# Performance work log

Measured on AMD Instinct MI355X. Metric: run time of the kernel, lower is better.

## Reference

```python
import jax, jax.numpy as jnp
import numpy as np

N = 20000          # nodes
E = 640000         # edges
IN_F, CL1_F, CL2_F, OUT_F = 128, 256, 128, 10
K = 4              # Chebyshev order
EPS = 1e-5         # BatchNorm eps
LAMBDA_MAX = 2.0   # PyG ChebConv default


def setup_inputs() -> dict:
    key = jax.random.key(0)
    ks = jax.random.split(key, 8)
    x = jax.random.normal(ks[0], (N, IN_F), dtype=jnp.float32)
    edge_index = jax.random.randint(ks[1], (2, E), 0, N, dtype=jnp.int64)
    edge_weight = jax.random.uniform(ks[2], (E,), dtype=jnp.float32)
    W1 = jax.random.normal(ks[3], (K, IN_F, CL1_F), dtype=jnp.float32) * 0.05
    b1 = jnp.zeros((CL1_F,), jnp.float32)
    W2 = jax.random.normal(ks[4], (K, CL1_F, CL2_F), dtype=jnp.float32) * 0.05
    b2 = jnp.zeros((CL2_F,), jnp.float32)
    gamma1 = jnp.ones((CL1_F,), jnp.float32); beta1 = jnp.zeros((CL1_F,), jnp.float32)
    gamma2 = jnp.ones((CL2_F,), jnp.float32); beta2 = jnp.zeros((CL2_F,), jnp.float32)
    Wlin = jax.random.normal(ks[5], (OUT_F, CL2_F), dtype=jnp.float32) * 0.05
    blin = jnp.zeros((OUT_F,), jnp.float32)
    return {"x": x, "edge_index": edge_index, "edge_weight": edge_weight,
            "W1": W1, "b1": b1, "W2": W2, "b2": b2,
            "gamma1": gamma1, "beta1": beta1, "gamma2": gamma2, "beta2": beta2,
            "Wlin": Wlin, "blin": blin}


def _cheb_norm(edge_index, edge_weight, n):
    # Scaled Laplacian L_hat = (2/lambda_max) * (I - D^{-1/2} A D^{-1/2}) - I
    # (matches PyG ChebConv __norm__ with normalization='sym').
    row, col = edge_index[0], edge_index[1]
    w = jnp.where(row == col, 0.0, edge_weight)  # remove_self_loops
    deg = jax.ops.segment_sum(w, row, num_segments=n)
    dis = jnp.where(deg > 0, 1.0 / jnp.sqrt(deg), 0.0)
    w_norm = -(dis[row] * w * dis[col]) * (2.0 / LAMBDA_MAX)
    diag_w = 2.0 / LAMBDA_MAX - 1.0  # = 0 for lambda_max=2
    return row, col, w_norm, diag_w


def _cheb_conv(x, row, col, w_norm, diag_w, W, b):
    n = x.shape[0]

    def spmm(t):  # L_hat @ t : gather sources, scale, scatter-add to targets
        return jax.ops.segment_sum(w_norm[:, None] * t[row], col, num_segments=n) + diag_w * t

    Tx0 = x
    out = Tx0 @ W[0]
    Tx1 = spmm(Tx0)
    out = out + Tx1 @ W[1]
    for k in range(2, W.shape[0]):  # Chebyshev recursion T_k = 2 L_hat T_{k-1} - T_{k-2}
        Tx2 = 2.0 * spmm(Tx1) - Tx0
        out = out + Tx2 @ W[k]
        Tx0, Tx1 = Tx1, Tx2
    return out + b


def _batchnorm(x, gamma, beta):  # training-mode BN over the node axis
    m = x.mean(axis=0)
    v = x.var(axis=0)
    return gamma * (x - m) / jnp.sqrt(v + EPS) + beta


def reference(x, edge_index, edge_weight, W1, b1, W2, b2,
              gamma1, beta1, gamma2, beta2, Wlin, blin):
    row, col, w_norm, diag_w = _cheb_norm(edge_index, edge_weight, x.shape[0])
    h = jax.nn.relu(_cheb_conv(x, row, col, w_norm, diag_w, W1, b1))
    h = _batchnorm(h, gamma1, beta1)
    h = jax.nn.relu(_cheb_conv(h, row, col, w_norm, diag_w, W2, b2))
    h = _batchnorm(h, gamma2, beta2)
    return h @ Wlin.T + blin  # [N, OUT_F]
```

## Files before the change

kernel.cpp:

```cpp
#include <hip/hip_runtime.h>
#include <cstdint>
#include <cstddef>

#define NNODES 20000
#define NEDGES 640000
#define IN_F   128
#define CL1_F  256
#define CL2_F  128
#define OUT_F  10
#define BN_EPS 1e-5f

#define NC     256
#define CE     (NEDGES / NC)
#define HALFN  10000

#define WB1    512
#define WB2    512
#define XB     ((NNODES * 16) / 256)

typedef unsigned short u16;


__device__ __forceinline__ float bf2f(u16 u) {
    union { uint32_t i; float f; } v; v.i = ((uint32_t)u) << 16; return v.f;
}
__device__ __forceinline__ u16 f2bf(float f) {
    union { float f; uint32_t i; } v; v.f = f;
    uint32_t r = v.i + 0x7fffu + ((v.i >> 16) & 1u);
    return (u16)(r >> 16);
}
__device__ __forceinline__ void bf2x2(uint32_t u, float& lo, float& hi) {
    union { uint32_t i; float f; } a, b;
    a.i = u << 16; b.i = u & 0xffff0000u;
    lo = a.f; hi = b.f;
}
__device__ __forceinline__ uint32_t f2bf2(float lo, float hi) {
    return (uint32_t)f2bf(lo) | ((uint32_t)f2bf(hi) << 16);
}
__device__ __forceinline__ void unpack8(uint4 v, float* o) {
    bf2x2(v.x, o[0], o[1]); bf2x2(v.y, o[2], o[3]);
    bf2x2(v.z, o[4], o[5]); bf2x2(v.w, o[6], o[7]);
}


__launch_bounds__(256)
__global__ void build_hist_conv(const int* __restrict__ ei, const float* __restrict__ ew,
                                u16* __restrict__ cnt_h, u16* __restrict__ degq_h,
                                const float* __restrict__ W1, u16* __restrict__ W1t,
                                const float* __restrict__ W2, u16* __restrict__ W2t,
                                const float* __restrict__ x, u16* __restrict__ A1,
                                int E, int N) {
    __shared__ uint32_t scnt[HALFN / 2];
    __shared__ uint32_t sdeg[HALFN / 2];
    int b = blockIdx.x;
    if (b < NC) {
        int e0 = b * CE, e1 = e0 + CE;
        for (int half = 0; half < 2; ++half) {
            int lo = half * HALFN;
            for (int i = threadIdx.x; i < HALFN / 2; i += 256) { scnt[i] = 0; sdeg[i] = 0; }
            __syncthreads();
            for (int e = e0 + threadIdx.x; e < e1; e += 256) {
                int r = ei[e];
                int c = ei[E + e];
                int ci = c - lo;
                if ((unsigned)ci < HALFN) atomicAdd(&scnt[ci >> 1], 1u << ((ci & 1) * 16));
                int ri = r - lo;
                if ((unsigned)ri < HALFN) {
                    float w = (r == c) ? 0.0f : ew[e];
                    uint32_t q = (uint32_t)(w * 1024.0f + 0.5f);
                    atomicAdd(&sdeg[ri >> 1], q << ((ri & 1) * 16));
                }
            }
            __syncthreads();
            for (int i = threadIdx.x; i < HALFN; i += 256) {
                cnt_h[(size_t)b * N + lo + i]  = (u16)((scnt[i >> 1] >> ((i & 1) * 16)) & 0xffffu);
                degq_h[(size_t)b * N + lo + i] = (u16)((sdeg[i >> 1] >> ((i & 1) * 16)) & 0xffffu);
            }
            __syncthreads();
        }
    } else {
        int b2 = b - NC;
        if (b2 < WB1) {
            int i = b2 * 256 + threadIdx.x;
            int k = i >> 8, n = i & 255;
            W1t[(size_t)n * 512 + k] = f2bf(W1[i]);
        } else if (b2 < WB1 + WB2) {
            int j = (b2 - WB1) * 256 + threadIdx.x;
            int kc = j / (256 * 128);
            int rem = j - kc * 256 * 128;
            int ci = rem >> 7, co = rem & 127;
            W2t[(size_t)(kc * 128 + co) * 256 + ci] = f2bf(W2[j]);
        } else {
            int j = (b2 - WB1 - WB2) * 256 + threadIdx.x;
            int n = j >> 4, f = (j & 15) << 3;
            const float4* xp = (const float4*)(x + (size_t)n * 128 + f);
            float4 v0 = xp[0], v1 = xp[1];
            uint4 o;
            o.x = f2bf2(v0.x, v0.y); o.y = f2bf2(v0.z, v0.w);
            o.z = f2bf2(v1.x, v1.y); o.w = f2bf2(v1.z, v1.w);
            *(uint4*)(A1 + (size_t)n * 512 + f) = o;
        }
    }
}

__global__ void reduce_dis_base(const u16* __restrict__ cnt_h, const u16* __restrict__ degq_h,
                                int* __restrict__ tot, float* __restrict__ dis,
                                u16* __restrict__ baseD, int N) {
    int i = blockIdx.x * blockDim.x + threadIdx.x;
    if (i >= N) return;
    int t = 0;
    uint32_t dq = 0;
#pragma unroll 8
    for (int c = 0; c < NC; ++c) {
        baseD[(size_t)c * N + i] = (u16)t;
        t  += cnt_h[(size_t)c * N + i];
        dq += degq_h[(size_t)c * N + i];
    }
    tot[i] = t;
    float d = (float)dq * (1.0f / 1024.0f);
    dis[i] = (d > 0.0f) ? rsqrtf(d) : 0.0f;
}


#define SCHUNK  80
#define SSTRIDE 81

__launch_bounds__(256)
__global__ void scan_kernel(const int* __restrict__ tot, int* __restrict__ rowptr, int N) {
    __shared__ int s[250 * SSTRIDE];
    __shared__ int wtot[4];
    int tid = threadIdx.x;

    const int4* t4 = (const int4*)tot;
    for (int i4 = tid; i4 < N / 4; i4 += 256) {
        int4 v = t4[i4];
        int i = i4 * 4;
        int c = i / SCHUNK;
        int idx = c * SSTRIDE + (i - c * SCHUNK);
        s[idx] = v.x; s[idx + 1] = v.y; s[idx + 2] = v.z; s[idx + 3] = v.w;
    }
    __syncthreads();

    int tsum = 0;
    if (tid < 250) {
        int base = tid * SSTRIDE;
#pragma unroll 8
        for (int j = 0; j < SCHUNK; ++j) tsum += s[base + j];
    }

    int lane = tid & 63, wv = tid >> 6;
    int pre = tsum;
#pragma unroll
    for (int off = 1; off < 64; off <<= 1) {
        int v = __shfl_up(pre, off);
        if (lane >= off) pre += v;
    }
    if (lane == 63) wtot[wv] = pre;
    __syncthreads();
    int run = pre - tsum;
    for (int w = 0; w < wv; ++w) run += wtot[w];
    if (tid == 0) rowptr[N] = wtot[0] + wtot[1] + wtot[2] + wtot[3];

    if (tid < 250) {
        int base = tid * SSTRIDE;
        for (int j = 0; j < SCHUNK; ++j) { int v = s[base + j]; s[base + j] = run; run += v; }
    }
    __syncthreads();

    int4* r4 = (int4*)rowptr;
    for (int i4 = tid; i4 < N / 4; i4 += 256) {
        int i = i4 * 4;
        int c = i / SCHUNK;
        int idx = c * SSTRIDE + (i - c * SCHUNK);
        int4 v;
        v.x = s[idx]; v.y = s[idx + 1]; v.z = s[idx + 2]; v.w = s[idx + 3];
        r4[i4] = v;
    }
}

__launch_bounds__(256)
__global__ void fill_kernel(const int* __restrict__ ei, const float* __restrict__ ew,
                            const float* __restrict__ dis, const int* __restrict__ rowptr,
                            const u16* __restrict__ baseD,
                            uint32_t* __restrict__ erec, int E, int N) {
    __shared__ uint32_t srank[NNODES / 2];
    int chunk = blockIdx.x;
    int e0 = chunk * CE, e1 = e0 + CE;
    for (int i = threadIdx.x; i < NNODES / 2; i += 256) srank[i] = 0;
    __syncthreads();
    for (int e = e0 + threadIdx.x; e < e1; e += 256) {
        int r = ei[e];
        int c = ei[E + e];
        float w = (r == c) ? 0.0f : ew[e];
        float wn = -(dis[r] * w * dis[c]);
        int sh = (c & 1) * 16;
        uint32_t old = atomicAdd(&srank[c >> 1], 1u << sh);
        int rank = (old >> sh) & 0xffff;
        int pos = rowptr[c] + (int)baseD[(size_t)chunk * N + c] + rank;
        erec[pos] = (uint32_t)r | ((uint32_t)f2bf(wn) << 16);
    }
}

__launch_bounds__(256)
__global__ void spmm_cl(const int* __restrict__ rowptr, const uint32_t* __restrict__ erec,
                        const u16* __restrict__ tin, int ldi,
                        const u16* __restrict__ t1, int ld1, float c1,
                        const u16* __restrict__ t2, int ld2, float c2,
                        u16* __restrict__ tout, int ldo,
                        const float* __restrict__ bias, int doReluBias,
                        int N, float s) {
    int gid = blockIdx.x * blockDim.x + threadIdx.x;
    int n = gid >> 4;
    if (n >= N) return;
    int f = (gid & 15) << 3;
    int p = rowptr[n], pe = rowptr[n + 1];
    float acc[8] = {};
    for (; p + 7 < pe; p += 8) {
        uint32_t rr[8];
#pragma unroll
        for (int u = 0; u < 8; ++u) rr[u] = erec[p + u];
        uint4 vv[8];
#pragma unroll
        for (int u = 0; u < 8; ++u)
            vv[u] = *(const uint4*)(tin + (size_t)(rr[u] & 0xffffu) * ldi + f);
#pragma unroll
        for (int u = 0; u < 8; ++u) {
            float w = bf2f((u16)(rr[u] >> 16));
            float fa[8];
            unpack8(vv[u], fa);
#pragma unroll
            for (int q = 0; q < 8; ++q) acc[q] += w * fa[q];
        }
    }
    for (; p < pe; ++p) {
        uint32_t r0 = erec[p];
        uint4 v0 = *(const uint4*)(tin + (size_t)(r0 & 0xffffu) * ldi + f);
        float w0 = bf2f((u16)(r0 >> 16));
        float fa[8];
        unpack8(v0, fa);
#pragma unroll
        for (int q = 0; q < 8; ++q) acc[q] += w0 * fa[q];
    }
#pragma unroll
    for (int q = 0; q < 8; ++q) acc[q] *= s;
    if (t1) {
        uint4 v = *(const uint4*)(t1 + (size_t)n * ld1 + f);
        float fv[8]; unpack8(v, fv);
#pragma unroll
        for (int q = 0; q < 8; ++q) acc[q] += c1 * fv[q];
    }
    if (t2) {
        uint4 v = *(const uint4*)(t2 + (size_t)n * ld2 + f);
        float fv[8]; unpack8(v, fv);
#pragma unroll
        for (int q = 0; q < 8; ++q) acc[q] += c2 * fv[q];
    }
    if (doReluBias) {
#pragma unroll
        for (int q = 0; q < 8; ++q) acc[q] = fmaxf(acc[q] + bias[f + q], 0.0f);
    }
    uint4 o;
    o.x = f2bf2(acc[0], acc[1]);
    o.y = f2bf2(acc[2], acc[3]);
    o.z = f2bf2(acc[4], acc[5]);
    o.w = f2bf2(acc[6], acc[7]);
    *(uint4*)(tout + (size_t)n * ldo + f) = o;
}


typedef __attribute__((ext_vector_type(8))) short short8;
typedef __attribute__((ext_vector_type(4))) float floatx4;

#define GBM 64
#define GBN 64
#define GBK 64

__launch_bounds__(256)
__global__ void gemm_mfma(const u16* __restrict__ A, const u16* __restrict__ Bt,
                          const float* __restrict__ bias, void* __restrict__ Cout,
                          float* __restrict__ ssum, float* __restrict__ ssq,
                          int M, int N, int K, int doRelu, int outBf) {
    __shared__ __align__(16) u16 As[GBM][GBK + 8];
    __shared__ __align__(16) u16 Bs[GBN][GBK + 8];
    __shared__ float colsum[GBN], colsq[GBN];

    int tid = threadIdx.x;
    int lane = tid & 63;
    int wave = tid >> 6;
    int wm = (wave & 1) * 32;
    int wn = (wave >> 1) * 32;
    int rowBase = blockIdx.x * GBM;
    int colBase = blockIdx.y * GBN;

    floatx4 acc[2][2];
#pragma unroll
    for (int i = 0; i < 2; ++i)
#pragma unroll
        for (int j = 0; j < 2; ++j) {
            acc[i][j][0] = 0.f; acc[i][j][1] = 0.f; acc[i][j][2] = 0.f; acc[i][j][3] = 0.f;
        }

    int sr = tid >> 3;
    int sc = (tid & 7) * 8;

    for (int k0 = 0; k0 < K; k0 += GBK) {
#pragma unroll
        for (int h = 0; h < 2; ++h) {
            int r = sr + h * 32;
            int gm = rowBase + r;
            uint4 v = make_uint4(0, 0, 0, 0);
            if (gm < M) v = *(const uint4*)(A + (size_t)gm * K + k0 + sc);
            *(uint4*)&As[r][sc] = v;
            int gn = colBase + r;
            uint4 w = *(const uint4*)(Bt + (size_t)gn * K + k0 + sc);
            *(uint4*)&Bs[r][sc] = w;
        }
        __syncthreads();

        int mrow = lane & 15;
        int kq = (lane >> 4) * 8;
#pragma unroll
        for (int kk = 0; kk < GBK; kk += 32) {
            short8 af[2], bfr[2];
#pragma unroll
            for (int i = 0; i < 2; ++i) af[i] = *(const short8*)&As[wm + i * 16 + mrow][kk + kq];
#pragma unroll
            for (int j = 0; j < 2; ++j) bfr[j] = *(const short8*)&Bs[wn + j * 16 + mrow][kk + kq];
#pragma unroll
            for (int i = 0; i < 2; ++i)
#pragma unroll
                for (int j = 0; j < 2; ++j)
                    acc[i][j] = __builtin_amdgcn_mfma_f32_16x16x32_bf16(af[i], bfr[j], acc[i][j], 0, 0, 0);
        }
        __syncthreads();
    }

    if (ssum) {
        if (tid < GBN) { colsum[tid] = 0.f; colsq[tid] = 0.f; }
        __syncthreads();
    }

    int cn0 = colBase + wn + (lane & 15);
    int rq = (lane >> 4) * 4;
    float* Cf = (float*)Cout;
    u16*   Cb = (u16*)Cout;
#pragma unroll
    for (int j = 0; j < 2; ++j) {
        float ps = 0.f, pq = 0.f;
        int n = cn0 + j * 16;
#pragma unroll
        for (int i = 0; i < 2; ++i) {
#pragma unroll
            for (int r = 0; r < 4; ++r) {
                int m = rowBase + wm + i * 16 + rq + r;
                if (m >= M) continue;
                float v = acc[i][j][r];
                if (bias) v += bias[n];
                if (doRelu) v = fmaxf(v, 0.0f);
                if (outBf) {
                    u16 bb = f2bf(v);
                    Cb[(size_t)m * N + n] = bb;
                    if (ssum) { float vb = bf2f(bb); ps += vb; pq += vb * vb; }
                } else {
                    Cf[(size_t)m * N + n] = v;
                }
            }
        }
        if (ssum) {
            int lc = wn + j * 16 + (lane & 15);
            atomicAdd(&colsum[lc], ps);
            atomicAdd(&colsq[lc], pq);
        }
    }
    if (ssum) {
        __syncthreads();
        if (tid < GBN) {
            atomicAdd(&ssum[colBase + tid], colsum[tid]);
            atomicAdd(&ssq[colBase + tid], colsq[tid]);
        }
    }
}


#define BN_ROWS 64
__global__ void bn_stats_bf(const u16* __restrict__ h, int N, int C,
                            float* __restrict__ sums, float* __restrict__ sumsq) {
    int c = threadIdx.x;
    int r0 = blockIdx.x * BN_ROWS;
    int r1 = min(r0 + BN_ROWS, N);
    float s = 0.f, q = 0.f;
    for (int r = r0; r < r1; ++r) {
        float v = bf2f(h[(size_t)r * C + c]);
        s += v;
        q += v * v;
    }
    atomicAdd(&sums[c], s);
    atomicAdd(&sumsq[c], q);
}

__launch_bounds__(256)
__global__ void fold_w2(u16* __restrict__ W2t, const float* __restrict__ sums,
                        const float* __restrict__ sumsq, const float* __restrict__ gamma,
                        const float* __restrict__ beta, float* __restrict__ rowvec, float invN) {
    __shared__ float red[4];
    int n = blockIdx.x;
    int k = threadIdx.x;
    float m = sums[k] * invN;
    float var = sumsq[k] * invN - m * m;
    float sc = gamma[k] / sqrtf(var + BN_EPS);
    float sh = beta[k] - m * sc;
    float wf = bf2f(W2t[(size_t)n * 256 + k]);
    W2t[(size_t)n * 256 + k] = f2bf(wf * sc);
    float part = sh * wf;
#pragma unroll
    for (int off = 32; off > 0; off >>= 1) part += __shfl_down(part, off);
    if ((k & 63) == 0) red[k >> 6] = part;
    __syncthreads();
    if (k == 0) rowvec[n] = red[0] + red[1] + red[2] + red[3];
}


__launch_bounds__(256)
__global__ void final_linear_bn(const u16* __restrict__ g, const float* __restrict__ Wlin,
                                const float* __restrict__ blin, const float* __restrict__ sums,
                                const float* __restrict__ sumsq, const float* __restrict__ gamma,
                                const float* __restrict__ beta, float* __restrict__ out,
                                int N, float invN) {
    __shared__ float Ws2[OUT_F][CL2_F + 4];
    __shared__ float scs[CL2_F], shs[CL2_F];
    __shared__ float oc[OUT_F];
    int tid = threadIdx.x;
    if (tid < CL2_F) {
        float m = sums[tid] * invN;
        float var = sumsq[tid] * invN - m * m;
        float sc = gamma[tid] / sqrtf(var + BN_EPS);
        scs[tid] = sc;
        shs[tid] = beta[tid] - m * sc;
    }
    __syncthreads();
    for (int i = tid; i < OUT_F * CL2_F; i += 256) {
        int f = i & 127;
        Ws2[i >> 7][f] = Wlin[i] * scs[f];
    }
    __syncthreads();
    if (tid < OUT_F) {
        float a = blin[tid];
        const float* wr = Wlin + tid * CL2_F;
        for (int f = 0; f < CL2_F; ++f) a += shs[f] * wr[f];
        oc[tid] = a;
    }
    __syncthreads();
    int idx = blockIdx.x * 256 + tid;
    if (idx >= N * OUT_F) return;
    int n = idx / OUT_F, o = idx - n * OUT_F;
    const u16* gr = g + (size_t)n * CL2_F;
    const float* w2 = Ws2[o];
    float acc = 0.f;
#pragma unroll
    for (int f0 = 0; f0 < CL2_F; f0 += 8) {
        uint4 v = *(const uint4*)(gr + f0);
        float fa[8]; unpack8(v, fa);
        const float4* wp = (const float4*)(w2 + f0);
        float4 wa = wp[0], wb = wp[1];
        acc += fa[0] * wa.x + fa[1] * wa.y + fa[2] * wa.z + fa[3] * wa.w
             + fa[4] * wb.x + fa[5] * wb.y + fa[6] * wb.z + fa[7] * wb.w;
    }
    out[idx] = acc + oc[o];
}


extern "C" void kernel_launch(void* const* d_in, const int* in_sizes, int n_in,
                              void* d_out, int out_size, void* d_ws, size_t ws_size,
                              hipStream_t stream) {
    const float* x      = (const float*)d_in[0];
    const int*   ei     = (const int*)d_in[1];
    const float* ew     = (const float*)d_in[2];
    const float* W1     = (const float*)d_in[3];
    const float* b1     = (const float*)d_in[4];
    const float* W2     = (const float*)d_in[5];
    const float* b2     = (const float*)d_in[6];
    const float* gamma1 = (const float*)d_in[7];
    const float* beta1  = (const float*)d_in[8];
    const float* gamma2 = (const float*)d_in[9];
    const float* beta2  = (const float*)d_in[10];
    const float* Wlin   = (const float*)d_in[11];
    const float* blin   = (const float*)d_in[12];
    float* out = (float*)d_out;

    const int N = NNODES, E = NEDGES;

    char* base = (char*)d_ws;
    u16*     cnt_h  = (u16*)    (base + 0);
    u16*     degq_h = (u16*)    (base + 10240000);
    u16*     baseD  = (u16*)    (base + 20480000);
    u16*     A1     = (u16*)    (base + 30720000);
    u16*     Hc     = A1;
    u16*     h1bf   = (u16*)    (base + 51200000);
    u16*     pbuf   = (u16*)    (base + 61440000);
    u16*     bb2    = (u16*)    (base + 66560000);
    u16*     bb1    = (u16*)    (base + 71680000);
    uint32_t* erec  = (uint32_t*)(base + 76800000);
    u16*     W1t    = (u16*)    (base + 79360000);
    u16*     W2t    = (u16*)    (base + 79622144);
    float*   rowvec = (float*)  (base + 79884288);
    int*     rowptr = (int*)    (base + 79886336);
    int*     tot    = (int*)    (base + 79966352);
    float*   dis    = (float*)  (base + 80046352);
    float*   bns1   = (float*)  (base + 80126352);
    float*   bnq1    = bns1 + 256;
    float*   bns2    = bnq1 + 256;
    float*   bnq2    = bns2 + 256;

    dim3 blk(256);

    hipMemsetAsync(bns1, 0, 4 * 256 * sizeof(float), stream);

    build_hist_conv<<<dim3(NC + WB1 + WB2 + XB), blk, 0, stream>>>(
        ei, ew, cnt_h, degq_h, W1, W1t, W2, W2t, x, A1, E, N);
    reduce_dis_base<<<dim3((N + 255) / 256), blk, 0, stream>>>(cnt_h, degq_h, tot, dis, baseD, N);
    scan_kernel<<<dim3(1), blk, 0, stream>>>(tot, rowptr, N);
    fill_kernel<<<dim3(NC), blk, 0, stream>>>(ei, ew, dis, rowptr, baseD, erec, E, N);

    dim3 gS(((N << 4) + 255) / 256);

    spmm_cl<<<gS, blk, 0, stream>>>(rowptr, erec, A1 + 0,   512, nullptr,  512, 0.f,
                                    nullptr, 512, 0.f, A1 + 128, 512, nullptr, 0, N, 1.0f);
    spmm_cl<<<gS, blk, 0, stream>>>(rowptr, erec, A1 + 128, 512, A1 + 0,   512, -1.f,
                                    nullptr, 512, 0.f, A1 + 256, 512, nullptr, 0, N, 2.0f);
    spmm_cl<<<gS, blk, 0, stream>>>(rowptr, erec, A1 + 256, 512, A1 + 128, 512, -1.f,
                                    nullptr, 512, 0.f, A1 + 384, 512, nullptr, 0, N, 2.0f);

    gemm_mfma<<<dim3((N + GBM - 1) / GBM, CL1_F / GBN), blk, 0, stream>>>(
        A1, W1t, b1, h1bf, bns1, bnq1, N, CL1_F, 512, 1, 1);

    fold_w2<<<dim3(512), dim3(256), 0, stream>>>(W2t, bns1, bnq1, gamma1, beta1, rowvec, 1.0f / N);

    gemm_mfma<<<dim3((N + GBM - 1) / GBM, 512 / GBN), blk, 0, stream>>>(
        h1bf, W2t, rowvec, Hc, nullptr, nullptr, N, 512, 256, 0, 1);

    spmm_cl<<<gS, blk, 0, stream>>>(rowptr, erec, Hc + 384, 512, Hc + 256, 512, 1.f,
                                    nullptr, 512, 0.f, bb2, 128, nullptr, 0, N, 2.0f);
    spmm_cl<<<gS, blk, 0, stream>>>(rowptr, erec, bb2, 128, Hc + 384, 512, -1.f,
                                    Hc + 128, 512, 1.f, bb1, 128, nullptr, 0, N, 2.0f);
    spmm_cl<<<gS, blk, 0, stream>>>(rowptr, erec, bb1, 128, bb2, 128, -1.f,
                                    Hc + 0, 512, 1.f, pbuf, 128, b2, 1, N, 1.0f);

    bn_stats_bf<<<dim3((N + BN_ROWS - 1) / BN_ROWS), dim3(CL2_F), 0, stream>>>(pbuf, N, CL2_F, bns2, bnq2);

    final_linear_bn<<<dim3((N * OUT_F + 255) / 256), blk, 0, stream>>>(
        pbuf, Wlin, blin, bns2, bnq2, gamma2, beta2, out, N, 1.0f / N);
}
```

Before: 349.6 us.

## Use float global atomics for degree, shuffle-shared edge loads in SpMM, vectorize BN stats

```diff
diff --git a/kernel.cpp b/kernel.cpp
--- a/kernel.cpp
+++ b/kernel.cpp
@@ -45,36 +45,31 @@
 
 __launch_bounds__(256)
 __global__ void build_hist_conv(const int* __restrict__ ei, const float* __restrict__ ew,
-                                u16* __restrict__ cnt_h, u16* __restrict__ degq_h,
+                                u16* __restrict__ cnt_h, float* __restrict__ degf,
                                 const float* __restrict__ W1, u16* __restrict__ W1t,
                                 const float* __restrict__ W2, u16* __restrict__ W2t,
                                 const float* __restrict__ x, u16* __restrict__ A1,
                                 int E, int N) {
     __shared__ uint32_t scnt[HALFN / 2];
-    __shared__ uint32_t sdeg[HALFN / 2];
     int b = blockIdx.x;
     if (b < NC) {
         int e0 = b * CE, e1 = e0 + CE;
         for (int half = 0; half < 2; ++half) {
             int lo = half * HALFN;
-            for (int i = threadIdx.x; i < HALFN / 2; i += 256) { scnt[i] = 0; sdeg[i] = 0; }
+            for (int i = threadIdx.x; i < HALFN / 2; i += 256) scnt[i] = 0;
             __syncthreads();
             for (int e = e0 + threadIdx.x; e < e1; e += 256) {
-                int r = ei[e];
                 int c = ei[E + e];
                 int ci = c - lo;
                 if ((unsigned)ci < HALFN) atomicAdd(&scnt[ci >> 1], 1u << ((ci & 1) * 16));
-                int ri = r - lo;
-                if ((unsigned)ri < HALFN) {
-                    float w = (r == c) ? 0.0f : ew[e];
-                    uint32_t q = (uint32_t)(w * 1024.0f + 0.5f);
-                    atomicAdd(&sdeg[ri >> 1], q << ((ri & 1) * 16));
+                if (half == 0) {
+                    int r = ei[e];
+                    if (r != c) atomicAdd(&degf[r], ew[e]);
                 }
             }
             __syncthreads();
             for (int i = threadIdx.x; i < HALFN; i += 256) {
-                cnt_h[(size_t)b * N + lo + i]  = (u16)((scnt[i >> 1] >> ((i & 1) * 16)) & 0xffffu);
-                degq_h[(size_t)b * N + lo + i] = (u16)((sdeg[i >> 1] >> ((i & 1) * 16)) & 0xffffu);
+                cnt_h[(size_t)b * N + lo + i] = (u16)((scnt[i >> 1] >> ((i & 1) * 16)) & 0xffffu);
             }
             __syncthreads();
         }
@@ -103,21 +98,19 @@
     }
 }
 
-__global__ void reduce_dis_base(const u16* __restrict__ cnt_h, const u16* __restrict__ degq_h,
+__global__ void reduce_dis_base(const u16* __restrict__ cnt_h, const float* __restrict__ degf,
                                 int* __restrict__ tot, float* __restrict__ dis,
                                 u16* __restrict__ baseD, int N) {
     int i = blockIdx.x * blockDim.x + threadIdx.x;
     if (i >= N) return;
     int t = 0;
-    uint32_t dq = 0;
 #pragma unroll 8
     for (int c = 0; c < NC; ++c) {
         baseD[(size_t)c * N + i] = (u16)t;
-        t  += cnt_h[(size_t)c * N + i];
-        dq += degq_h[(size_t)c * N + i];
+        t += cnt_h[(size_t)c * N + i];
     }
     tot[i] = t;
-    float d = (float)dq * (1.0f / 1024.0f);
+    float d = degf[i];
     dis[i] = (d > 0.0f) ? rsqrtf(d) : 0.0f;
 }
 
@@ -213,8 +206,32 @@
     int n = gid >> 4;
     if (n >= N) return;
     int f = (gid & 15) << 3;
+    int sub = gid & 15;
+    int gbase = threadIdx.x & 48;
     int p = rowptr[n], pe = rowptr[n + 1];
     float acc[8] = {};
+    for (; p + 15 < pe; p += 16) {
+        uint32_t myrec = erec[p + sub];
+#pragma unroll
+        for (int h = 0; h < 2; ++h) {
+            uint32_t rr[8];
+#pragma unroll
+            for (int u = 0; u < 8; ++u)
+                rr[u] = (uint32_t)__shfl((int)myrec, gbase + h * 8 + u, 64);
+            uint4 vv[8];
+#pragma unroll
+            for (int u = 0; u < 8; ++u)
+                vv[u] = *(const uint4*)(tin + (size_t)(rr[u] & 0xffffu) * ldi + f);
+#pragma unroll
+            for (int u = 0; u < 8; ++u) {
+                float w = bf2f((u16)(rr[u] >> 16));
+                float fa[8];
+                unpack8(vv[u], fa);
+#pragma unroll
+                for (int q = 0; q < 8; ++q) acc[q] += w * fa[q];
+            }
+        }
+    }
     for (; p + 7 < pe; p += 8) {
         uint32_t rr[8];
 #pragma unroll
@@ -382,20 +399,43 @@
 }
 
 
-#define BN_ROWS 64
-__global__ void bn_stats_bf(const u16* __restrict__ h, int N, int C,
+__launch_bounds__(256)
+__global__ void bn_stats_bf(const u16* __restrict__ h, int N,
                             float* __restrict__ sums, float* __restrict__ sumsq) {
-    int c = threadIdx.x;
-    int r0 = blockIdx.x * BN_ROWS;
-    int r1 = min(r0 + BN_ROWS, N);
-    float s = 0.f, q = 0.f;
-    for (int r = r0; r < r1; ++r) {
-        float v = bf2f(h[(size_t)r * C + c]);
-        s += v;
-        q += v * v;
-    }
-    atomicAdd(&sums[c], s);
-    atomicAdd(&sumsq[c], q);
+    __shared__ float reds[4][16][8];
+    __shared__ float redq[4][16][8];
+    int tid = threadIdx.x;
+    int co = (tid & 15) << 3;
+    int rg = tid >> 4;
+    int r = blockIdx.x * 64 + rg;
+    float s[8] = {}, q[8] = {};
+#pragma unroll
+    for (int i = 0; i < 4; ++i, r += 16) {
+        if (r < N) {
+            uint4 v = *(const uint4*)(h + (size_t)r * CL2_F + co);
+            float fa[8]; unpack8(v, fa);
+#pragma unroll
+            for (int j = 0; j < 8; ++j) { s[j] += fa[j]; q[j] += fa[j] * fa[j]; }
+        }
+    }
+#pragma unroll
+    for (int j = 0; j < 8; ++j) {
+        s[j] += __shfl_xor(s[j], 16); s[j] += __shfl_xor(s[j], 32);
+        q[j] += __shfl_xor(q[j], 16); q[j] += __shfl_xor(q[j], 32);
+    }
+    int wv = tid >> 6, ln = tid & 63;
+    if (ln < 16) {
+#pragma unroll
+        for (int j = 0; j < 8; ++j) { reds[wv][ln][j] = s[j]; redq[wv][ln][j] = q[j]; }
+    }
+    __syncthreads();
+    if (tid < 128) {
+        int g = tid >> 3, j = tid & 7;
+        float ss = reds[0][g][j] + reds[1][g][j] + reds[2][g][j] + reds[3][g][j];
+        float qq = redq[0][g][j] + redq[1][g][j] + redq[2][g][j] + redq[3][g][j];
+        atomicAdd(&sums[(g << 3) + j], ss);
+        atomicAdd(&sumsq[(g << 3) + j], qq);
+    }
 }
 
 __launch_bounds__(256)
@@ -491,7 +531,11 @@
 
     char* base = (char*)d_ws;
     u16*     cnt_h  = (u16*)    (base + 0);
-    u16*     degq_h = (u16*)    (base + 10240000);
+    float*   degf   = (float*)  (base + 10240000);
+    float*   bns1   = (float*)  (base + 10320000);
+    float*   bnq1   = bns1 + 256;
+    float*   bns2   = bnq1 + 256;
+    float*   bnq2   = bns2 + 256;
     u16*     baseD  = (u16*)    (base + 20480000);
     u16*     A1     = (u16*)    (base + 30720000);
     u16*     Hc     = A1;
@@ -506,18 +550,14 @@
     int*     rowptr = (int*)    (base + 79886336);
     int*     tot    = (int*)    (base + 79966352);
     float*   dis    = (float*)  (base + 80046352);
-    float*   bns1   = (float*)  (base + 80126352);
-    float*   bnq1    = bns1 + 256;
-    float*   bns2    = bnq1 + 256;
-    float*   bnq2    = bns2 + 256;
 
     dim3 blk(256);
 
-    hipMemsetAsync(bns1, 0, 4 * 256 * sizeof(float), stream);
+    hipMemsetAsync(degf, 0, N * sizeof(float) + 4 * 256 * sizeof(float), stream);
 
     build_hist_conv<<<dim3(NC + WB1 + WB2 + XB), blk, 0, stream>>>(
-        ei, ew, cnt_h, degq_h, W1, W1t, W2, W2t, x, A1, E, N);
-    reduce_dis_base<<<dim3((N + 255) / 256), blk, 0, stream>>>(cnt_h, degq_h, tot, dis, baseD, N);
+        ei, ew, cnt_h, degf, W1, W1t, W2, W2t, x, A1, E, N);
+    reduce_dis_base<<<dim3((N + 255) / 256), blk, 0, stream>>>(cnt_h, degf, tot, dis, baseD, N);
     scan_kernel<<<dim3(1), blk, 0, stream>>>(tot, rowptr, N);
     fill_kernel<<<dim3(NC), blk, 0, stream>>>(ei, ew, dis, rowptr, baseD, erec, E, N);
 
@@ -545,7 +585,7 @@
     spmm_cl<<<gS, blk, 0, stream>>>(rowptr, erec, bb1, 128, bb2, 128, -1.f,
                                     Hc + 0, 512, 1.f, pbuf, 128, b2, 1, N, 1.0f);
 
-    bn_stats_bf<<<dim3((N + BN_ROWS - 1) / BN_ROWS), dim3(CL2_F), 0, stream>>>(pbuf, N, CL2_F, bns2, bnq2);
+    bn_stats_bf<<<dim3((N + 63) / 64, 1), blk, 0, stream>>>(pbuf, N, bns2, bnq2);
 
     final_linear_bn<<<dim3((N * OUT_F + 255) / 256), blk, 0, stream>>>(
         pbuf, Wlin, blin, bns2, bnq2, gamma2, beta2, out, N, 1.0f / N);
```

After: 423.8 us. 21.2% more time.
